# Performance work log

Hardware: AMD Instinct MI355X
Metric: run time of the kernel (lower is better)

## Reference

```python
import jax, jax.numpy as jnp
import numpy as np

N_NODES = 100000
N_EDGES = 1000000
DIM_IN = 64
DIM_OUT = 64


def setup_inputs() -> dict:
    key = jax.random.key(0)
    k1, k2, k3 = jax.random.split(key, 3)
    x = jax.random.normal(k1, (N_NODES, DIM_IN), dtype=jnp.float32)
    W = jax.random.normal(k2, (DIM_OUT, DIM_IN), dtype=jnp.float32) * (1.0 / np.sqrt(DIM_IN))
    edge_index = jax.random.randint(k3, (2, N_EDGES), 0, N_NODES, dtype=jnp.int64)
    return {"x": x, "W": W, "edge_index": edge_index, "K": 3}


def _gcn_norm(edge_index, num_nodes):
    # add self-loops with weight 1 (PyG gcn_norm default)
    loop = jnp.arange(num_nodes, dtype=edge_index.dtype)
    src = jnp.concatenate([edge_index[0], loop])
    dst = jnp.concatenate([edge_index[1], loop])
    w = jnp.ones(src.shape[0], dtype=jnp.float32)
    deg = jax.ops.segment_sum(w, dst, num_segments=num_nodes)  # degree on col/dst
    dinv = jnp.where(deg > 0, jax.lax.rsqrt(deg), 0.0)
    norm = dinv[src] * w * dinv[dst]  # D^-1/2 A_hat D^-1/2 edge weights
    return src, dst, norm


def reference(x, W, edge_index, K):
    n = x.shape[0]
    src, dst, norm = _gcn_norm(edge_index, n)
    # K-hop propagation: x <- sum_{(s,d)} norm * x[s] into d
    for _ in range(K):
        x = jax.ops.segment_sum(norm[:, None] * x[src], dst, num_segments=n)
    # Linear, bias=False (dropout is identity in eval mode)
    return x @ W.T
```

## Files before the change

### kernel.cpp

```cpp
#include <hip/hip_runtime.h>
#include <hip/hip_fp16.h>
#include <stdint.h>

#define N_NODES 100000
#define N_EDGES 1000000
#define DIM 64
#define MAXD 32
#define SENT N_NODES
#define BKT_SHIFT 7
#define BKT_NODES 128
#define NBKT ((N_NODES + BKT_NODES - 1) / BKT_NODES)
#define BKT_CAP 2048
#define OVF_CAP 16384
#define CHUNK 2048
#define NCHUNK ((N_EDGES + CHUNK - 1) / CHUNK)
#define CURS_STRIDE 16
#define LROWS 64

__device__ __forceinline__ int load_src(const void* edges, int is64, int e) {
    if (is64) return ((const int2*)edges)[e].x;
    return ((const int*)edges)[e];
}
__device__ __forceinline__ int load_dst(const void* edges, int is64, int e) {
    if (is64) return ((const int2*)edges)[N_EDGES + e].x;
    return ((const int*)edges)[N_EDGES + e];
}

__global__ void init_kernel(const void* __restrict__ edges, int* __restrict__ flag,
                            int* __restrict__ cnt, int* __restrict__ ovf_cnt) {
    int i = blockIdx.x * blockDim.x + threadIdx.x;
    if (i < N_NODES) cnt[i] = 0;
    if (i == 0) {
        *ovf_cnt = 0;
        const long long* e64 = (const long long*)edges;
        int is64 = 1;
        for (int k = 0; k < 8; ++k) {
            long long v = e64[k];
            if (v < 0 || v >= (long long)N_NODES) is64 = 0;
        }
        *flag = is64;
    }
}

__global__ __launch_bounds__(256) void hist_kernel(const void* __restrict__ edges,
                                                   const int* __restrict__ flag,
                                                   int* __restrict__ hist) {
    __shared__ int lcnt[NBKT];
    int t = threadIdx.x;
    int e0 = blockIdx.x * CHUNK;
    int e1 = min(e0 + CHUNK, N_EDGES);
    int is64 = *flag;
    for (int i = t; i < NBKT; i += 256) lcnt[i] = 0;
    __syncthreads();
    for (int e = e0 + t; e < e1; e += 256)
        atomicAdd(&lcnt[load_dst(edges, is64, e) >> BKT_SHIFT], 1);
    __syncthreads();
    int* row = hist + (size_t)blockIdx.x * NBKT;
    for (int i = t; i < NBKT; i += 256) row[i] = lcnt[i];
}

__global__ __launch_bounds__(256) void scan_kernel(int* __restrict__ hist,
                                                   int* __restrict__ cursors) {
    int b = blockIdx.x * 4 + (threadIdx.x >> 6);
    if (b >= NBKT) return;
    int lane = threadIdx.x & 63;
    int carry = 0;
    for (int r0 = 0; r0 < NCHUNK; r0 += 64) {
        int r = r0 + lane;
        int v = (r < NCHUNK) ? hist[(size_t)r * NBKT + b] : 0;
        int incl = v;
#pragma unroll
        for (int off = 1; off < 64; off <<= 1) {
            int u = __shfl_up(incl, off, 64);
            if (lane >= off) incl += u;
        }
        if (r < NCHUNK) hist[(size_t)r * NBKT + b] = incl - v + carry;
        carry += __shfl(incl, 63, 64);
    }
    if (lane == 0) cursors[b * CURS_STRIDE] = carry;
}

__global__ __launch_bounds__(256) void scatter2(const void* __restrict__ edges,
                                                const int* __restrict__ flag,
                                                const int* __restrict__ hist,
                                                int* __restrict__ cnt,
                                                int* __restrict__ buckets,
                                                int2* __restrict__ ovf,
                                                int* __restrict__ ovf_cnt) {
    __shared__ int lbase[NBKT];
    __shared__ int lcur[NBKT];
    int t = threadIdx.x;
    int e0 = blockIdx.x * CHUNK;
    int e1 = min(e0 + CHUNK, N_EDGES);
    int is64 = *flag;
    const int* row = hist + (size_t)blockIdx.x * NBKT;
    for (int i = t; i < NBKT; i += 256) { lbase[i] = row[i]; lcur[i] = 0; }
    __syncthreads();
    for (int e = e0 + t; e < e1; e += 256) {
        int s = load_src(edges, is64, e);
        int d = load_dst(edges, is64, e);
        int b = d >> BKT_SHIFT;
        int pos = lbase[b] + atomicAdd(&lcur[b], 1);
        if (pos < BKT_CAP) {
            buckets[(size_t)b * BKT_CAP + pos] = s | ((d & (BKT_NODES - 1)) << 17);
        } else {
            atomicAdd(&cnt[d], 1);
            int o = atomicAdd(ovf_cnt, 1);
            if (o < OVF_CAP) ovf[o] = make_int2(s, d);
        }
    }
}

__global__ __launch_bounds__(256) void ell_build(const int* __restrict__ cursors,
                                                 int* __restrict__ cnt,
                                                 int* __restrict__ ellcnt,
                                                 float* __restrict__ dinv,
                                                 const int* __restrict__ buckets,
                                                 int* __restrict__ ell,
                                                 int2* __restrict__ ovf,
                                                 int* __restrict__ ovf_cnt) {
    __shared__ int lcnt[BKT_NODES];
    int b = blockIdx.x, t = threadIdx.x;
    if (t < BKT_NODES) lcnt[t] = 0;
    __syncthreads();
    int m = cursors[b * CURS_STRIDE];
    if (m > BKT_CAP) m = BKT_CAP;
    int base = b * BKT_NODES;
    const int* be = buckets + (size_t)b * BKT_CAP;
    for (int i = t; i < m; i += 256) {
        int pe = be[i];
        int s = pe & 0x1FFFF;
        int off = pe >> 17;
        int k = atomicAdd(&lcnt[off], 1);
        if (k < MAXD) ell[(size_t)(base + off) * MAXD + k] = s;
        else {
            int o = atomicAdd(ovf_cnt, 1);
            if (o < OVF_CAP) ovf[o] = make_int2(s, base + off);
        }
    }
    __syncthreads();
    if (t < BKT_NODES) {
        int g = base + t;
        if (g < N_NODES) {
            int tot = cnt[g] + lcnt[t];
            cnt[g] = tot;
            int ec = lcnt[t] < MAXD ? lcnt[t] : MAXD;
            ellcnt[g] = ec;
            dinv[g] = rsqrtf((float)(tot + 1));
            int pe4 = (ec + 3) & ~3;
            if (pe4 > MAXD) pe4 = MAXD;
            for (int k = ec; k < pe4; ++k)
                ell[(size_t)g * MAXD + k] = SENT;
        }
    }
}

__global__ void vinit_h(const float* __restrict__ x, const float* __restrict__ dinv,
                        __half* __restrict__ xh, __half* __restrict__ bA,
                        __half* __restrict__ bB) {
    int i = blockIdx.x * blockDim.x + threadIdx.x;
    if (blockIdx.x == 0 && threadIdx.x < 96) {
        int r = threadIdx.x >> 5, c = threadIdx.x & 31;
        __half* bufs[3] = {xh, bA, bB};
        ((__half2*)(bufs[r] + (size_t)SENT * DIM))[c] = __floats2half2_rn(0.f, 0.f);
    }
    if (i >= N_NODES * DIM / 4) return;
    int node = i >> 4;
    float dv = dinv[node];
    float4 v = ((const float4*)x)[i];
    __half2* o = (__half2*)(xh + (size_t)i * 4);
    o[0] = __floats2half2_rn(dv * v.x, dv * v.y);
    o[1] = __floats2half2_rn(dv * v.z, dv * v.w);
}

template <int FINAL>
__global__ __launch_bounds__(256) void hop_kernel(const __half* __restrict__ vin,
                                                  const int* __restrict__ ellcnt,
                                                  const int* __restrict__ ell,
                                                  const float* __restrict__ dinv,
                                                  const int2* __restrict__ ovf,
                                                  const int* __restrict__ ovf_cnt,
                                                  __half* __restrict__ y) {
    int t = blockIdx.x * blockDim.x + threadIdx.x;
    int n = t >> 6;
    if (n >= N_NODES) return;
    int d = t & 63;
    int deg4 = (ellcnt[n] + 3) & ~3;
    int idx = ell[(n << 5) + (d & 31)];
    float dn = dinv[n];
    float acc = __half2float(vin[(size_t)n * DIM + d]);
    int j = 0;
    for (; j + 8 <= deg4; j += 8) {
#pragma unroll
        for (int kk = 0; kk < 8; ++kk) {
            int s = __shfl(idx, j + kk, 64);
            acc += __half2float(vin[(size_t)s * DIM + d]);
        }
    }
    if (j < deg4) {
#pragma unroll
        for (int kk = 0; kk < 4; ++kk) {
            int s = __shfl(idx, j + kk, 64);
            acc += __half2float(vin[(size_t)s * DIM + d]);
        }
    }
    int m = *ovf_cnt;
    if (m > OVF_CAP) m = OVF_CAP;
    for (int i = 0; i < m; ++i) {
        int2 e = ovf[i];
        if (e.y == n) acc += __half2float(vin[(size_t)e.x * DIM + d]);
    }
    float scale = FINAL ? dn : dn * dn;
    y[(size_t)n * DIM + d] = __float2half(scale * acc);
}

__global__ __launch_bounds__(256) void linear_kernel(const __half* __restrict__ xin,
                                                     const float* __restrict__ W,
                                                     float* __restrict__ out) {
    __shared__ float sx[LROWS * DIM];
    int tid = threadIdx.x;
    size_t row0 = (size_t)blockIdx.x * LROWS;

    for (int it = 0; it < 4; ++it) {
        int i = tid + it * 256;
        int r = i >> 4, kc = i & 15;
        size_t gr = row0 + r;
        if (gr >= N_NODES) gr = N_NODES - 1;
        const __half2* hp = (const __half2*)&xin[gr * DIM + kc * 4];
        float2 f0 = __half22float2(hp[0]);
        float2 f1 = __half22float2(hp[1]);
        int kcs = kc ^ (r & 7);
        *(float4*)&sx[r * DIM + kcs * 4] = make_float4(f0.x, f0.y, f1.x, f1.y);
    }
    __syncthreads();

    int lane = tid & 63;
    int wv = __builtin_amdgcn_readfirstlane(tid >> 6);
    float4 xr[16];
#pragma unroll
    for (int kc = 0; kc < 16; ++kc) {
        int kcs = kc ^ (lane & 7);
        xr[kc] = *(const float4*)&sx[lane * DIM + kcs * 4];
    }

    float a[4][4];
#pragma unroll
    for (int cc = 0; cc < 4; ++cc)
#pragma unroll
        for (int jj = 0; jj < 4; ++jj) a[cc][jj] = 0.f;

    int c0base = wv * 16;
#pragma unroll
    for (int cc = 0; cc < 4; ++cc) {
        int c0 = c0base + cc * 4;
        const float* __restrict__ w0 = W + (size_t)(c0 + 0) * DIM;
        const float* __restrict__ w1 = W + (size_t)(c0 + 1) * DIM;
        const float* __restrict__ w2 = W + (size_t)(c0 + 2) * DIM;
        const float* __restrict__ w3 = W + (size_t)(c0 + 3) * DIM;
#pragma unroll
        for (int q = 0; q < 16; ++q) {
            float xk[4] = {xr[q].x, xr[q].y, xr[q].z, xr[q].w};
#pragma unroll
            for (int u = 0; u < 4; ++u) {
                int k = q * 4 + u;
                a[cc][0] = fmaf(xk[u], w0[k], a[cc][0]);
                a[cc][1] = fmaf(xk[u], w1[k], a[cc][1]);
                a[cc][2] = fmaf(xk[u], w2[k], a[cc][2]);
                a[cc][3] = fmaf(xk[u], w3[k], a[cc][3]);
            }
        }
    }

    __syncthreads();
#pragma unroll
    for (int cc = 0; cc < 4; ++cc) {
        int chunk = wv * 4 + cc;
        int cs = chunk ^ (lane & 7);
        *(float4*)&sx[lane * DIM + cs * 4] =
            make_float4(a[cc][0], a[cc][1], a[cc][2], a[cc][3]);
    }
    __syncthreads();
    for (int it = 0; it < 4; ++it) {
        int i = tid + it * 256;
        int r = i >> 4, kc = i & 15;
        size_t gr = row0 + r;
        if (gr < N_NODES) {
            int kcs = kc ^ (r & 7);
            *(float4*)&out[gr * DIM + kc * 4] = *(const float4*)&sx[r * DIM + kcs * 4];
        }
    }
}

extern "C" void kernel_launch(void* const* d_in, const int* in_sizes, int n_in,
                              void* d_out, int out_size, void* d_ws, size_t ws_size,
                              hipStream_t stream) {
    const float* x     = (const float*)d_in[0];
    const float* W     = (const float*)d_in[1];
    const void*  edges = d_in[2];
    float* out = (float*)d_out;

    char* ws = (char*)d_ws;
    int*    flag    = (int*)(ws + 0);
    int*    ovf_cnt = (int*)(ws + 4);
    int*    cursors = (int*)(ws + 4096);
    int*    cnt     = (int*)(ws + 65536);
    int*    ellcnt  = (int*)(ws + 465536);
    float*  dinv    = (float*)(ws + 865536);
    int2*   ovf     = (int2*)(ws + 1265536);
    int*    ell     = (int*)(ws + 1396608);
    __half* xh      = (__half*)(ws + 14196608);
    __half* bufHA   = (__half*)(ws + 27000832);
    __half* bufHB   = (__half*)(ws + 39804928);
    int*    buckets = (int*)(ws + 39804928);
    int*    hist    = (int*)(ws + 52609024);

    const int NB = (N_NODES + 255) / 256;
    const int HB = (N_NODES * 64 + 255) / 256;
    const int VB = (N_NODES * DIM / 4 + 255) / 256;
    const int LB = (N_NODES + LROWS - 1) / LROWS;
    const int SB = (NBKT + 3) / 4;

    init_kernel<<<NB, 256, 0, stream>>>(edges, flag, cnt, ovf_cnt);
    hist_kernel<<<NCHUNK, 256, 0, stream>>>(edges, flag, hist);
    scan_kernel<<<SB, 256, 0, stream>>>(hist, cursors);
    scatter2<<<NCHUNK, 256, 0, stream>>>(edges, flag, hist, cnt, buckets, ovf, ovf_cnt);
    ell_build<<<NBKT, 256, 0, stream>>>(cursors, cnt, ellcnt, dinv, buckets, ell, ovf, ovf_cnt);

    vinit_h<<<VB, 256, 0, stream>>>(x, dinv, xh, bufHA, bufHB);
    hop_kernel<0><<<HB, 256, 0, stream>>>(xh,    ellcnt, ell, dinv, ovf, ovf_cnt, bufHB);
    hop_kernel<0><<<HB, 256, 0, stream>>>(bufHB, ellcnt, ell, dinv, ovf, ovf_cnt, bufHA);
    hop_kernel<1><<<HB, 256, 0, stream>>>(bufHA, ellcnt, ell, dinv, ovf, ovf_cnt, bufHB);

    linear_kernel<<<LB, 256, 0, stream>>>(bufHB, W, out);
}
```

Before: 156.4 us.

## Process two nodes per wavefront with half2 gathers and pair-padded ELL rows

The hop kernel now maps each 64-lane wavefront to two nodes, with every lane gathering a __half2 (two features) per neighbor. This halves the thread count and doubles bytes per load. Each half-wave loops to the larger padded degree of the pair. ELL rows are therefore padded with sentinel entries up to the multiple of 8 covering the neighbor node's degree. The edge chunk size for the histogram/scatter is also doubled. The cost is extra sentinel gathers when the paired degrees differ.

```diff
diff --git a/kernel.cpp b/kernel.cpp
--- a/kernel.cpp
+++ b/kernel.cpp
@@ -12,7 +12,7 @@
 #define NBKT ((N_NODES + BKT_NODES - 1) / BKT_NODES)
 #define BKT_CAP 2048
 #define OVF_CAP 16384
-#define CHUNK 2048
+#define CHUNK 4096
 #define NCHUNK ((N_EDGES + CHUNK - 1) / CHUNK)
 #define CURS_STRIDE 16
 #define LROWS 64
@@ -147,9 +147,11 @@
             int ec = lcnt[t] < MAXD ? lcnt[t] : MAXD;
             ellcnt[g] = ec;
             dinv[g] = rsqrtf((float)(tot + 1));
-            int pe4 = (ec + 3) & ~3;
-            if (pe4 > MAXD) pe4 = MAXD;
-            for (int k = ec; k < pe4; ++k)
+            int ecn = lcnt[t ^ 1] < MAXD ? lcnt[t ^ 1] : MAXD;
+            int mx = ec > ecn ? ec : ecn;
+            int pe8 = (mx + 7) & ~7;
+            if (pe8 > MAXD) pe8 = MAXD;
+            for (int k = ec; k < pe8; ++k)
                 ell[(size_t)g * MAXD + k] = SENT;
         }
     }
@@ -182,36 +184,39 @@
                                                   const int* __restrict__ ovf_cnt,
                                                   __half* __restrict__ y) {
     int t = blockIdx.x * blockDim.x + threadIdx.x;
-    int n = t >> 6;
+    int lane = t & 63;
+    int l5 = lane & 31;
+    int n = ((t >> 6) << 1) + (lane >> 5);
     if (n >= N_NODES) return;
-    int d = t & 63;
-    int deg4 = (ellcnt[n] + 3) & ~3;
-    int idx = ell[(n << 5) + (d & 31)];
+    int deg8 = (ellcnt[n] + 7) & ~7;
+    int dther = __shfl_xor(deg8, 32, 64);
+    int dmax = deg8 > dther ? deg8 : dther;
+    int idx = ell[(n << 5) + l5];
     float dn = dinv[n];
-    float acc = __half2float(vin[(size_t)n * DIM + d]);
-    int j = 0;
-    for (; j + 8 <= deg4; j += 8) {
+    const __half2* v2 = (const __half2*)vin;
+    float2 sf = __half22float2(v2[(size_t)(n << 5) + l5]);
+    float accx = sf.x, accy = sf.y;
+    int orv = lane & 32;
+    for (int j = 0; j < dmax; j += 8) {
 #pragma unroll
         for (int kk = 0; kk < 8; ++kk) {
-            int s = __shfl(idx, j + kk, 64);
-            acc += __half2float(vin[(size_t)s * DIM + d]);
-        }
-    }
-    if (j < deg4) {
-#pragma unroll
-        for (int kk = 0; kk < 4; ++kk) {
-            int s = __shfl(idx, j + kk, 64);
-            acc += __half2float(vin[(size_t)s * DIM + d]);
+            int s = __shfl(idx, (j + kk) | orv, 64);
+            float2 gf = __half22float2(v2[(size_t)(s << 5) + l5]);
+            accx += gf.x;
+            accy += gf.y;
         }
     }
     int m = *ovf_cnt;
     if (m > OVF_CAP) m = OVF_CAP;
     for (int i = 0; i < m; ++i) {
         int2 e = ovf[i];
-        if (e.y == n) acc += __half2float(vin[(size_t)e.x * DIM + d]);
+        if (e.y == n) {
+            float2 gf = __half22float2(v2[(size_t)(e.x << 5) + l5]);
+            accx += gf.x; accy += gf.y;
+        }
     }
     float scale = FINAL ? dn : dn * dn;
-    y[(size_t)n * DIM + d] = __float2half(scale * acc);
+    ((__half2*)y)[(size_t)(n << 5) + l5] = __floats2half2_rn(scale * accx, scale * accy);
 }
 
 __global__ __launch_bounds__(256) void linear_kernel(const __half* __restrict__ xin,
@@ -315,7 +320,7 @@
     int*    hist    = (int*)(ws + 52609024);
 
     const int NB = (N_NODES + 255) / 256;
-    const int HB = (N_NODES * 64 + 255) / 256;
+    const int HB = ((N_NODES + 1) / 2 * 64 + 255) / 256;
     const int VB = (N_NODES * DIM / 4 + 255) / 256;
     const int LB = (N_NODES + LROWS - 1) / LROWS;
     const int SB = (NBKT + 3) / 4;
```

New measurement: 143.8 us. 8.1% less time.
